# Optimization experiments

Hardware: AMD Instinct MI355X
Metric: run time of the kernel (lower is better)

## Reference

```python
import jax, jax.numpy as jnp
import numpy as np

N_LEVELS = 16
NFPL = 2
LOG2_T = 19
TABLE_SIZE = 1 << LOG2_T
BASE_RES = 16.0
FINEST_RES = 512.0
N_POINTS = 1048576

# hash primes from HashNeRF's hash() (xor of coord*prime per axis)
PRIMES = jnp.array([1, 2654435761, 805459861], dtype=jnp.uint32)
# corner offsets: index = 4*i + 2*j + k (i outermost), matching BOX_OFFSETS
OFFSETS = jnp.array([[i, j, k] for i in (0, 1) for j in (0, 1) for k in (0, 1)], dtype=jnp.int32)  # [8,3]


def setup_inputs() -> dict:
    key = jax.random.key(0)
    k1, k2 = jax.random.split(key)
    x = jax.random.uniform(k1, (N_POINTS, 3), dtype=jnp.float32)  # points in [0,1)^3
    # nn.Embedding tables init uniform(-1e-4, 1e-4), stacked over levels
    tables = jax.random.uniform(k2, (N_LEVELS, TABLE_SIZE, NFPL), minval=-1e-4, maxval=1e-4, dtype=jnp.float32)
    return {"x": x, "tables": tables}


def _level_embed(x, table, resolution):
    # x: [N,3] in box [0,1]^3; table: [T,F]; resolution: scalar float
    grid = 1.0 / resolution
    xc = jnp.clip(x, 0.0, 1.0)
    bl = jnp.floor(xc / grid).astype(jnp.int32)            # [N,3] bottom-left voxel idx
    vmin = bl.astype(jnp.float32) * grid                    # voxel_min_vertex
    vmax = vmin + grid                                      # voxel_max_vertex
    corners = bl[:, None, :] + OFFSETS[None, :, :]          # [N,8,3]
    h = corners.astype(jnp.uint32) * PRIMES                 # wrap-around uint32 mult
    idx = (h[..., 0] ^ h[..., 1] ^ h[..., 2]) & jnp.uint32(TABLE_SIZE - 1)  # [N,8]
    emb = table[idx.astype(jnp.int32)]                      # [N,8,F] gather
    # trilinear interp (weights use unclamped x as in the original)
    w = (x - vmin) / (vmax - vmin)                          # [N,3]
    w0, w1, w2 = w[:, 0:1], w[:, 1:2], w[:, 2:3]
    c00 = emb[:, 0] * (1 - w0) + emb[:, 4] * w0
    c01 = emb[:, 1] * (1 - w0) + emb[:, 5] * w0
    c10 = emb[:, 2] * (1 - w0) + emb[:, 6] * w0
    c11 = emb[:, 3] * (1 - w0) + emb[:, 7] * w0
    c0 = c00 * (1 - w1) + c10 * w1
    c1 = c01 * (1 - w1) + c11 * w1
    return c0 * (1 - w2) + c1 * w2                          # [N,F]


def reference(x, tables):
    b = np.exp((np.log(FINEST_RES) - np.log(BASE_RES)) / (N_LEVELS - 1))
    res = jnp.floor(BASE_RES * (b ** jnp.arange(N_LEVELS, dtype=jnp.float32)))  # [L]
    feats = jax.vmap(_level_embed, in_axes=(None, 0, 0))(x, tables, res)        # [L,N,F]
    out = jnp.moveaxis(feats, 0, 1).reshape(x.shape[0], N_LEVELS * NFPL)        # [N,32]
    # original: if last dim != 16, F.pad(x, (0, 16 - D)); negative pad crops
    D = out.shape[-1]
    if D > 16:
        out = out[:, :16]
    elif D < 16:
        out = jnp.pad(out, ((0, 0), (0, 16 - D)))
    return out
```

## Files before the change

### kernel.cpp

```cpp
#include <hip/hip_runtime.h>
#include <hip/hip_fp16.h>
#include <stdint.h>


#define TABLE_SIZE (1u << 19)
#define TMASK (TABLE_SIZE - 1u)
#define P2 2654435761u
#define P3 805459861u

#define FSCALE 8192.0f
#define FINV   1.220703125e-4f

#define QUAD_BYTES_OFF 262144
#define PAIR_BYTES_OFF 16777216

#define OFF_Q3 0
#define OFF_Q4 33792
#define OFF_Q5 99392
#define OFF_Q6 226892

__device__ __forceinline__ void quad_geom(int l, float& R, int& DK, int& offq) {
    switch (l) {
        case 3: R=32.f; DK=32; offq=OFF_Q3; break;
        case 4: R=40.f; DK=40; offq=OFF_Q4; break;
        case 5: R=50.f; DK=50; offq=OFF_Q5; break;
        default:R=64.f; DK=64; offq=OFF_Q6; break;
    }
}

__device__ __forceinline__ uint32_t pack_s(float a, float b) {
    __half2 h = __floats2half2_rn(a * FSCALE, b * FSCALE);
    return *(uint32_t*)&h;
}
__device__ __forceinline__ uint32_t pack_r(float a, float b) {
    __half2 h = __floats2half2_rn(a, b);
    return *(uint32_t*)&h;
}
__device__ __forceinline__ float2 h2f(uint32_t u) {
    __half2 h = *(__half2*)&u;
    return __half22float2(h);
}
__device__ __forceinline__ uint32_t getc(const uint4 v, int k) {
    return k == 0 ? v.x : k == 1 ? v.y : k == 2 ? v.z : v.w;
}

__global__ __launch_bounds__(256) void build_tables_kernel(
    const float* __restrict__ tables, float2* __restrict__ dense,
    uint4* __restrict__ quads, uint2* __restrict__ pairs)
{
    const int role = (int)blockIdx.y;
    const int e = (int)blockIdx.x * 256 + (int)threadIdx.x;

    if (role < 4) {
        float Rf; int DK, offq;
        quad_geom(3 + role, Rf, DK, offq);
        const int l = 3 + role;
        const int E = (DK + 1) * DK * DK;
        if (e >= E) return;
        const int d2 = DK * DK;
        const int i = e / d2;
        const int rem = e - i * d2;
        const int j = rem / DK;
        const int k = rem - j * DK;
        const float2* __restrict__ tab = (const float2*)tables + (size_t)l * (size_t)TABLE_SIZE;
        const uint32_t hx  = (uint32_t)i;
        const uint32_t hy0 = (uint32_t)j * P2, hy1 = hy0 + P2;
        const uint32_t hz0 = (uint32_t)k * P3, hz1 = hz0 + P3;
        const float2 v00 = tab[(hx ^ hy0 ^ hz0) & TMASK];
        const float2 v01 = tab[(hx ^ hy0 ^ hz1) & TMASK];
        const float2 v10 = tab[(hx ^ hy1 ^ hz0) & TMASK];
        const float2 v11 = tab[(hx ^ hy1 ^ hz1) & TMASK];
        uint4 u;
        u.x = pack_s(v00.x, v00.y);
        u.y = pack_s(v01.x, v01.y);
        u.z = pack_s(v10.x, v10.y);
        u.w = pack_s(v11.x, v11.y);
        quads[offq + e] = u;
    } else if (role == 4) {
        const int E = 81 * 81 * 80;
        if (e >= E) return;
        const int i = e / 6480;
        const int rem = e - i * 6480;
        const int j = rem / 80;
        const int k = rem - j * 80;
        const float2* __restrict__ tab = (const float2*)tables + (size_t)7 * (size_t)TABLE_SIZE;
        const uint32_t hb = (uint32_t)i ^ ((uint32_t)j * P2);
        const float2 a = tab[(hb ^ ((uint32_t)k * P3)) & TMASK];
        const float2 b = tab[(hb ^ ((uint32_t)(k + 1) * P3)) & TMASK];
        uint2 u;
        u.x = pack_s(a.x, a.y);
        u.y = pack_s(b.x, b.y);
        pairs[e] = u;
    } else {
        if (e >= 31750) return;
        int lv, DIM, off;
        if (e < 4913)       { lv = 0; DIM = 17; off = 0; }
        else if (e < 14174) { lv = 1; DIM = 21; off = 4913; }
        else                { lv = 2; DIM = 26; off = 14174; }
        const int le = e - off;
        const int d2 = DIM * DIM;
        const int i = le / d2;
        const int rem = le - i * d2;
        const int j = rem / DIM;
        const int k = rem - j * DIM;
        const uint32_t h = ((uint32_t)i ^ ((uint32_t)j * P2) ^ ((uint32_t)k * P3)) & TMASK;
        const float2* __restrict__ tab = (const float2*)tables + (size_t)lv * (size_t)TABLE_SIZE;
        dense[e] = tab[h];
    }
}

__device__ uint32_t embed_quad_one(int l, const uint4* __restrict__ quads,
                                   float px, float py, float pz) {
    float R; int DK, offq;
    quad_geom(l, R, DK, offq);
    const float g = 1.0f / R;
    const float cx = fminf(fmaxf(px, 0.0f), 1.0f);
    const float cy = fminf(fmaxf(py, 0.0f), 1.0f);
    const float cz = fminf(fmaxf(pz, 0.0f), 1.0f);
    const int bx = min((int)floorf(cx * R), DK - 1);
    const int by = min((int)floorf(cy * R), DK - 1);
    const int bz = min((int)floorf(cz * R), DK - 1);
    const float wx = (px - (float)bx * g) * R;
    const float wy = (py - (float)by * g) * R;
    const float wz = (pz - (float)bz * g) * R;
    const int d2 = DK * DK;
    const int idx = (bx * DK + by) * DK + bz;
    const uint4 qa = quads[offq + idx];
    const uint4 qb = quads[offq + idx + d2];
    const float omx = 1.0f - wx, omy = 1.0f - wy, omz = 1.0f - wz;
    const float2 a00 = h2f(qa.x), a01 = h2f(qa.y), a10 = h2f(qa.z), a11 = h2f(qa.w);
    const float2 b00 = h2f(qb.x), b01 = h2f(qb.y), b10 = h2f(qb.z), b11 = h2f(qb.w);
    const float m00a = a00.x*omx + b00.x*wx, m00b = a00.y*omx + b00.y*wx;
    const float m01a = a01.x*omx + b01.x*wx, m01b = a01.y*omx + b01.y*wx;
    const float m10a = a10.x*omx + b10.x*wx, m10b = a10.y*omx + b10.y*wx;
    const float m11a = a11.x*omx + b11.x*wx, m11b = a11.y*omx + b11.y*wx;
    const float c0a = m00a*omz + m01a*wz, c0b = m00b*omz + m01b*wz;
    const float c1a = m10a*omz + m11a*wz, c1b = m10b*omz + m11b*wz;
    return pack_r(c0a*omy + c1a*wy, c0b*omy + c1b*wy);
}
__device__ uint32_t embed_pair7_one(const uint2* __restrict__ pairs,
                                    float px, float py, float pz) {
    const float R = 80.f, g = 1.0f / R;
    const float cx = fminf(fmaxf(px, 0.0f), 1.0f);
    const float cy = fminf(fmaxf(py, 0.0f), 1.0f);
    const float cz = fminf(fmaxf(pz, 0.0f), 1.0f);
    const int bx = min((int)floorf(cx * R), 79);
    const int by = min((int)floorf(cy * R), 79);
    const int bz = min((int)floorf(cz * R), 79);
    const float wx = (px - (float)bx * g) * R;
    const float wy = (py - (float)by * g) * R;
    const float wz = (pz - (float)bz * g) * R;
    const int idx = (bx * 81 + by) * 80 + bz;
    const uint2 d00 = pairs[idx];
    const uint2 d01 = pairs[idx + 80];
    const uint2 d10 = pairs[idx + 6480];
    const uint2 d11 = pairs[idx + 6560];
    const float omx = 1.0f - wx, omy = 1.0f - wy, omz = 1.0f - wz;
    const float2 a00 = h2f(d00.x), z00 = h2f(d00.y);
    const float2 a01 = h2f(d01.x), z01 = h2f(d01.y);
    const float2 a10 = h2f(d10.x), z10 = h2f(d10.y);
    const float2 a11 = h2f(d11.x), z11 = h2f(d11.y);
    const float c00a = a00.x*omz + z00.x*wz, c00b = a00.y*omz + z00.y*wz;
    const float c01a = a01.x*omz + z01.x*wz, c01b = a01.y*omz + z01.y*wz;
    const float c10a = a10.x*omz + z10.x*wz, c10b = a10.y*omz + z10.y*wz;
    const float c11a = a11.x*omz + z11.x*wz, c11b = a11.y*omz + z11.y*wz;
    const float e0a = c00a*omy + c01a*wy, e0b = c00b*omy + c01b*wy;
    const float e1a = c10a*omy + c11a*wy, e1b = c10b*omy + c11b*wy;
    return pack_r(e0a*omx + e1a*wx, e0b*omx + e1b*wx);
}

__global__ __launch_bounds__(256, 4) void embed_levels_kernel(
    const float* __restrict__ x, const uint4* __restrict__ quads,
    const uint2* __restrict__ pairs, uint32_t* __restrict__ wsh,
    int n, int bpl)
{
    const int bid = (int)blockIdx.x;
    const int q = bid / bpl;
    const int l = 3 + q;
    const int pb = bid - q * bpl;
    const int p0 = pb * 1024 + 4 * (int)threadIdx.x;
    if (p0 >= n) return;

    uint32_t* __restrict__ wl = wsh + (size_t)l * (size_t)n;

    if (p0 + 4 > n) {
        for (int pp = 0; pp < 4; ++pp) {
            const int i = p0 + pp;
            if (i >= n) break;
            const float px = x[3*i], py = x[3*i+1], pz = x[3*i+2];
            wl[i] = (l < 7) ? embed_quad_one(l, quads, px, py, pz)
                            : embed_pair7_one(pairs, px, py, pz);
        }
        return;
    }

    const float4* __restrict__ xv = (const float4*)(x + (size_t)3 * p0);
    const float4 f0 = xv[0], f1 = xv[1], f2 = xv[2];
    const float px0 = f0.x, py0 = f0.y, pz0 = f0.z;
    const float px1 = f0.w, py1 = f1.x, pz1 = f1.y;
    const float px2 = f1.z, py2 = f1.w, pz2 = f2.x;
    const float px3 = f2.y, py3 = f2.z, pz3 = f2.w;

    uint32_t r0, r1, r2, r3;

    if (l < 7) {
        float R; int DK, offq;
        quad_geom(l, R, DK, offq);
        const float g = 1.0f / R;
        const int bmax = DK - 1;
        const int d2 = DK * DK;
        const uint4* __restrict__ tab = quads + offq;

#define QPREP(k) \
        const float cx##k = fminf(fmaxf(px##k, 0.0f), 1.0f); \
        const float cy##k = fminf(fmaxf(py##k, 0.0f), 1.0f); \
        const float cz##k = fminf(fmaxf(pz##k, 0.0f), 1.0f); \
        const int bx##k = min((int)floorf(cx##k * R), bmax); \
        const int by##k = min((int)floorf(cy##k * R), bmax); \
        const int bz##k = min((int)floorf(cz##k * R), bmax); \
        const float wx##k = (px##k - (float)bx##k * g) * R; \
        const float wy##k = (py##k - (float)by##k * g) * R; \
        const float wz##k = (pz##k - (float)bz##k * g) * R; \
        const int ia##k = (bx##k * DK + by##k) * DK + bz##k; \
        const int ib##k = ia##k + d2;

        QPREP(0) QPREP(1) QPREP(2) QPREP(3)

#define QGATHER(k) \
        const uint4 qa##k = tab[ia##k]; \
        const uint4 qb##k = tab[ib##k];

        QGATHER(0) QGATHER(1) QGATHER(2) QGATHER(3)

#define QINTERP(k, dst) { \
        const float omx = 1.0f - wx##k, omy = 1.0f - wy##k, omz = 1.0f - wz##k; \
        const float2 a00 = h2f(qa##k.x), a01 = h2f(qa##k.y); \
        const float2 a10 = h2f(qa##k.z), a11 = h2f(qa##k.w); \
        const float2 b00 = h2f(qb##k.x), b01 = h2f(qb##k.y); \
        const float2 b10 = h2f(qb##k.z), b11 = h2f(qb##k.w); \
        const float m00a = a00.x*omx + b00.x*wx##k, m00b = a00.y*omx + b00.y*wx##k; \
        const float m01a = a01.x*omx + b01.x*wx##k, m01b = a01.y*omx + b01.y*wx##k; \
        const float m10a = a10.x*omx + b10.x*wx##k, m10b = a10.y*omx + b10.y*wx##k; \
        const float m11a = a11.x*omx + b11.x*wx##k, m11b = a11.y*omx + b11.y*wx##k; \
        const float c0a = m00a*omz + m01a*wz##k, c0b = m00b*omz + m01b*wz##k; \
        const float c1a = m10a*omz + m11a*wz##k, c1b = m10b*omz + m11b*wz##k; \
        dst = pack_r(c0a*omy + c1a*wy##k, c0b*omy + c1b*wy##k); }

        QINTERP(0, r0) QINTERP(1, r1) QINTERP(2, r2) QINTERP(3, r3)
    } else {
        const float R = 80.f, g = 1.0f / R;

#define SPREP(k) \
        const float cx##k = fminf(fmaxf(px##k, 0.0f), 1.0f); \
        const float cy##k = fminf(fmaxf(py##k, 0.0f), 1.0f); \
        const float cz##k = fminf(fmaxf(pz##k, 0.0f), 1.0f); \
        const int bx##k = min((int)floorf(cx##k * R), 79); \
        const int by##k = min((int)floorf(cy##k * R), 79); \
        const int bz##k = min((int)floorf(cz##k * R), 79); \
        const float wx##k = (px##k - (float)bx##k * g) * R; \
        const float wy##k = (py##k - (float)by##k * g) * R; \
        const float wz##k = (pz##k - (float)bz##k * g) * R; \
        const int ix##k = (bx##k * 81 + by##k) * 80 + bz##k;

        SPREP(0) SPREP(1) SPREP(2) SPREP(3)

#define SGATHER(k) \
        const uint2 d00##k = pairs[ix##k]; \
        const uint2 d01##k = pairs[ix##k + 80]; \
        const uint2 d10##k = pairs[ix##k + 6480]; \
        const uint2 d11##k = pairs[ix##k + 6560];

        SGATHER(0) SGATHER(1) SGATHER(2) SGATHER(3)

#define SINTERP(k, dst) { \
        const float omx = 1.0f - wx##k, omy = 1.0f - wy##k, omz = 1.0f - wz##k; \
        const float2 a00 = h2f(d00##k.x), z00 = h2f(d00##k.y); \
        const float2 a01 = h2f(d01##k.x), z01 = h2f(d01##k.y); \
        const float2 a10 = h2f(d10##k.x), z10 = h2f(d10##k.y); \
        const float2 a11 = h2f(d11##k.x), z11 = h2f(d11##k.y); \
        const float c00a = a00.x*omz + z00.x*wz##k, c00b = a00.y*omz + z00.y*wz##k; \
        const float c01a = a01.x*omz + z01.x*wz##k, c01b = a01.y*omz + z01.y*wz##k; \
        const float c10a = a10.x*omz + z10.x*wz##k, c10b = a10.y*omz + z10.y*wz##k; \
        const float c11a = a11.x*omz + z11.x*wz##k, c11b = a11.y*omz + z11.y*wz##k; \
        const float e0a = c00a*omy + c01a*wy##k, e0b = c00b*omy + c01b*wy##k; \
        const float e1a = c10a*omy + c11a*wy##k, e1b = c10b*omy + c11b*wy##k; \
        dst = pack_r(e0a*omx + e1a*wx##k, e0b*omx + e1b*wx##k); }

        SINTERP(0, r0) SINTERP(1, r1) SINTERP(2, r2) SINTERP(3, r3)
    }

    *(uint4*)(wl + p0) = make_uint4(r0, r1, r2, r3);
}

__global__ __launch_bounds__(1024) void embed_lds_kernel(
    const float* __restrict__ x, const float2* __restrict__ dense,
    uint32_t* __restrict__ wsh, int n, int lv, int DIM, int E, int doff)
{
    extern __shared__ float2 lds[];
    for (int e = (int)threadIdx.x; e < E; e += 1024) lds[e] = dense[doff + e];
    __syncthreads();

    const int p0 = ((int)blockIdx.x * 1024 + (int)threadIdx.x) * 4;
    if (p0 >= n) return;

    const float R = (lv == 0) ? 16.f : (lv == 1) ? 20.f : 25.f;
    const float g = 1.0f / R;
    const int D2 = DIM * DIM;
    const int bmax = DIM - 2;

    float px[4], py[4], pz[4];
    if (p0 + 4 <= n) {
        const float4* __restrict__ xv = (const float4*)(x + (size_t)3 * p0);
        const float4 f0 = xv[0], f1 = xv[1], f2 = xv[2];
        px[0] = f0.x; py[0] = f0.y; pz[0] = f0.z;
        px[1] = f0.w; py[1] = f1.x; pz[1] = f1.y;
        px[2] = f1.z; py[2] = f1.w; pz[2] = f2.x;
        px[3] = f2.y; py[3] = f2.z; pz[3] = f2.w;
    } else {
#pragma unroll
        for (int k = 0; k < 4; ++k) {
            const int i = min(p0 + k, n - 1);
            px[k] = x[3*i]; py[k] = x[3*i+1]; pz[k] = x[3*i+2];
        }
    }

    uint32_t r[4];
#pragma unroll
    for (int k = 0; k < 4; ++k) {
        const float cx = fminf(fmaxf(px[k], 0.0f), 1.0f);
        const float cy = fminf(fmaxf(py[k], 0.0f), 1.0f);
        const float cz = fminf(fmaxf(pz[k], 0.0f), 1.0f);
        const int bx = min((int)floorf(cx * R), bmax);
        const int by = min((int)floorf(cy * R), bmax);
        const int bz = min((int)floorf(cz * R), bmax);
        const float wx = (px[k] - (float)bx * g) * R;
        const float wy = (py[k] - (float)by * g) * R;
        const float wz = (pz[k] - (float)bz * g) * R;
        const int c = (bx * DIM + by) * DIM + bz;
        const float2 e000 = lds[c];
        const float2 e001 = lds[c + 1];
        const float2 e010 = lds[c + DIM];
        const float2 e011 = lds[c + DIM + 1];
        const float2 e100 = lds[c + D2];
        const float2 e101 = lds[c + D2 + 1];
        const float2 e110 = lds[c + D2 + DIM];
        const float2 e111 = lds[c + D2 + DIM + 1];
        const float omx = 1.0f - wx, omy = 1.0f - wy, omz = 1.0f - wz;
        const float c00a = e000.x*omx + e100.x*wx, c00b = e000.y*omx + e100.y*wx;
        const float c01a = e001.x*omx + e101.x*wx, c01b = e001.y*omx + e101.y*wx;
        const float c10a = e010.x*omx + e110.x*wx, c10b = e010.y*omx + e110.y*wx;
        const float c11a = e011.x*omx + e111.x*wx, c11b = e011.y*omx + e111.y*wx;
        const float c0a = c00a*omy + c10a*wy, c0b = c00b*omy + c10b*wy;
        const float c1a = c01a*omy + c11a*wy, c1b = c01b*omy + c11b*wy;
        r[k] = pack_s(c0a*omz + c1a*wz, c0b*omz + c1b*wz);
    }
    if (p0 + 4 <= n) {
        *(uint4*)(wsh + (size_t)lv * n + p0) = make_uint4(r[0], r[1], r[2], r[3]);
    } else {
        for (int k = 0; k < 4 && p0 + k < n; ++k)
            wsh[(size_t)lv * n + p0 + k] = r[k];
    }
}

__global__ __launch_bounds__(256) void aos_kernel(
    const uint32_t* __restrict__ wsh, float* __restrict__ out, int n)
{
    const int p0 = ((int)blockIdx.x * 256 + (int)threadIdx.x) * 4;
    if (p0 >= n) return;

    if (p0 + 4 <= n) {
        const uint4 v0 = *(const uint4*)(wsh + 0 * (size_t)n + p0);
        const uint4 v1 = *(const uint4*)(wsh + 1 * (size_t)n + p0);
        const uint4 v2 = *(const uint4*)(wsh + 2 * (size_t)n + p0);
        const uint4 v3 = *(const uint4*)(wsh + 3 * (size_t)n + p0);
        const uint4 v4 = *(const uint4*)(wsh + 4 * (size_t)n + p0);
        const uint4 v5 = *(const uint4*)(wsh + 5 * (size_t)n + p0);
        const uint4 v6 = *(const uint4*)(wsh + 6 * (size_t)n + p0);
        const uint4 v7 = *(const uint4*)(wsh + 7 * (size_t)n + p0);
#pragma unroll
        for (int k = 0; k < 4; ++k) {
            const float2 f0 = h2f(getc(v0, k)), f1 = h2f(getc(v1, k));
            const float2 f2 = h2f(getc(v2, k)), f3 = h2f(getc(v3, k));
            const float2 f4 = h2f(getc(v4, k)), f5 = h2f(getc(v5, k));
            const float2 f6 = h2f(getc(v6, k)), f7 = h2f(getc(v7, k));
            float4* __restrict__ op = (float4*)(out + (size_t)(p0 + k) * 16);
            op[0] = make_float4(f0.x*FINV, f0.y*FINV, f1.x*FINV, f1.y*FINV);
            op[1] = make_float4(f2.x*FINV, f2.y*FINV, f3.x*FINV, f3.y*FINV);
            op[2] = make_float4(f4.x*FINV, f4.y*FINV, f5.x*FINV, f5.y*FINV);
            op[3] = make_float4(f6.x*FINV, f6.y*FINV, f7.x*FINV, f7.y*FINV);
        }
    } else {
        for (int k = 0; k < 4 && p0 + k < n; ++k) {
            const int i = p0 + k;
            float* __restrict__ op = out + (size_t)i * 16;
#pragma unroll
            for (int l = 0; l < 8; ++l) {
                const float2 f = h2f(wsh[(size_t)l * n + i]);
                op[2*l + 0] = f.x * FINV;
                op[2*l + 1] = f.y * FINV;
            }
        }
    }
}

__global__ __launch_bounds__(256) void hash_embed_mono_kernel(
    const float* __restrict__ x, const float* __restrict__ tables,
    float* __restrict__ out, int n)
{
    const int i = blockIdx.x * 256 + threadIdx.x;
    if (i >= n) return;
    const float px = x[3*i+0], py = x[3*i+1], pz = x[3*i+2];
    const float cx = fminf(fmaxf(px, 0.0f), 1.0f);
    const float cy = fminf(fmaxf(py, 0.0f), 1.0f);
    const float cz = fminf(fmaxf(pz, 0.0f), 1.0f);
    const float resf[8] = {16.f,20.f,25.f,32.f,40.f,50.f,64.f,80.f};
    float o[16];
#pragma unroll
    for (int l = 0; l < 8; ++l) {
        const float R = resf[l], g = 1.0f / R;
        const int bx = (int)floorf(cx*R), by = (int)floorf(cy*R), bz = (int)floorf(cz*R);
        const float wx = (px - bx*g)*R, wy = (py - by*g)*R, wz = (pz - bz*g)*R;
        const uint32_t hx0 = (uint32_t)bx, hx1 = hx0+1u;
        const uint32_t hy0 = (uint32_t)by*P2, hy1 = hy0+P2;
        const uint32_t hz0 = (uint32_t)bz*P3, hz1 = hz0+P3;
        const float2* tab = (const float2*)(tables) + (size_t)l*(size_t)TABLE_SIZE;
        const float2 e000 = tab[(hx0^hy0^hz0)&TMASK], e001 = tab[(hx0^hy0^hz1)&TMASK];
        const float2 e010 = tab[(hx0^hy1^hz0)&TMASK], e011 = tab[(hx0^hy1^hz1)&TMASK];
        const float2 e100 = tab[(hx1^hy0^hz0)&TMASK], e101 = tab[(hx1^hy0^hz1)&TMASK];
        const float2 e110 = tab[(hx1^hy1^hz0)&TMASK], e111 = tab[(hx1^hy1^hz1)&TMASK];
        const float omx = 1.f-wx, omy = 1.f-wy, omz = 1.f-wz;
        const float c00a = e000.x*omx + e100.x*wx, c00b = e000.y*omx + e100.y*wx;
        const float c01a = e001.x*omx + e101.x*wx, c01b = e001.y*omx + e101.y*wx;
        const float c10a = e010.x*omx + e110.x*wx, c10b = e010.y*omx + e110.y*wx;
        const float c11a = e011.x*omx + e111.x*wx, c11b = e011.y*omx + e111.y*wx;
        const float c0a = c00a*omy + c10a*wy, c0b = c00b*omy + c10b*wy;
        const float c1a = c01a*omy + c11a*wy, c1b = c01b*omy + c11b*wy;
        o[2*l+0] = c0a*omz + c1a*wz;
        o[2*l+1] = c0b*omz + c1b*wz;
    }
    float4* op = (float4*)(out + (size_t)i * 16);
    op[0] = make_float4(o[0],o[1],o[2],o[3]);
    op[1] = make_float4(o[4],o[5],o[6],o[7]);
    op[2] = make_float4(o[8],o[9],o[10],o[11]);
    op[3] = make_float4(o[12],o[13],o[14],o[15]);
}

extern "C" void kernel_launch(void* const* d_in, const int* in_sizes, int n_in,
                              void* d_out, int out_size, void* d_ws, size_t ws_size,
                              hipStream_t stream) {
    const float* x = (const float*)d_in[0];
    const float* tables = (const float*)d_in[1];
    float* out = (float*)d_out;
    const int n = in_sizes[0] / 3;

    static int cap = -1;
    if (cap < 0) {
        cap = (hipFuncSetAttribute((const void*)embed_lds_kernel,
                  hipFuncAttributeMaxDynamicSharedMemorySize, 140608) == hipSuccess)
              ? 1 : 0;
    }
    const size_t ws_needed = (size_t)8 * (size_t)n * sizeof(uint32_t);
    if (ws_size < ws_needed || cap == 0) {
        hash_embed_mono_kernel<<<(n + 255) / 256, 256, 0, stream>>>(x, tables, out, n);
        return;
    }

    uint32_t* wsh = (uint32_t*)d_ws;
    float2* dense = (float2*)out;
    uint4*  quads = (uint4*)((char*)out + QUAD_BYTES_OFF);
    uint2*  pairs = (uint2*)((char*)out + PAIR_BYTES_OFF);

    build_tables_kernel<<<dim3(2051, 6), 256, 0, stream>>>(tables, dense, quads, pairs);

    static const int DIMt[3] = {17, 21, 26};
    static const int Et[3]   = {4913, 9261, 17576};
    static const int OFFt[3] = {0, 4913, 14174};
    const int lgrid = (n + 4095) / 4096;
    for (int lv = 0; lv < 3; ++lv) {
        embed_lds_kernel<<<lgrid, 1024, (size_t)Et[lv] * sizeof(float2), stream>>>(
            x, dense, wsh, n, lv, DIMt[lv], Et[lv], OFFt[lv]);
    }

    const int bpl = (n + 1023) / 1024;
    embed_levels_kernel<<<5 * bpl, 256, 0, stream>>>(x, quads, pairs, wsh, n, bpl);

    aos_kernel<<<(n + 1023) / 1024, 256, 0, stream>>>(wsh, out, n);
}
```

Before: 255.5 us.

## Fuse coarse dense levels into output kernel and move level 2 to quad path

```diff
diff --git a/kernel.cpp b/kernel.cpp
--- a/kernel.cpp
+++ b/kernel.cpp
@@ -14,13 +14,19 @@
 #define QUAD_BYTES_OFF 262144
 #define PAIR_BYTES_OFF 16777216
 
-#define OFF_Q3 0
-#define OFF_Q4 33792
-#define OFF_Q5 99392
-#define OFF_Q6 226892
+#define OFF_Q2 0
+#define OFF_Q3 16250
+#define OFF_Q4 50042
+#define OFF_Q5 115642
+#define OFF_Q6 243142
+
+#define DENSE_L1_OFF 4913
+#define DENSE_E 14174
+#define DENSE_BYTES (DENSE_E * 8)
 
 __device__ __forceinline__ void quad_geom(int l, float& R, int& DK, int& offq) {
     switch (l) {
+        case 2: R=25.f; DK=25; offq=OFF_Q2; break;
         case 3: R=32.f; DK=32; offq=OFF_Q3; break;
         case 4: R=40.f; DK=40; offq=OFF_Q4; break;
         case 5: R=50.f; DK=50; offq=OFF_Q5; break;
@@ -51,10 +57,10 @@
     const int role = (int)blockIdx.y;
     const int e = (int)blockIdx.x * 256 + (int)threadIdx.x;
 
-    if (role < 4) {
+    if (role < 5) {
         float Rf; int DK, offq;
-        quad_geom(3 + role, Rf, DK, offq);
-        const int l = 3 + role;
+        quad_geom(2 + role, Rf, DK, offq);
+        const int l = 2 + role;
         const int E = (DK + 1) * DK * DK;
         if (e >= E) return;
         const int d2 = DK * DK;
@@ -76,7 +82,7 @@
         u.z = pack_s(v10.x, v10.y);
         u.w = pack_s(v11.x, v11.y);
         quads[offq + e] = u;
-    } else if (role == 4) {
+    } else if (role == 5) {
         const int E = 81 * 81 * 80;
         if (e >= E) return;
         const int i = e / 6480;
@@ -92,11 +98,10 @@
         u.y = pack_s(b.x, b.y);
         pairs[e] = u;
     } else {
-        if (e >= 31750) return;
+        if (e >= DENSE_E) return;
         int lv, DIM, off;
-        if (e < 4913)       { lv = 0; DIM = 17; off = 0; }
-        else if (e < 14174) { lv = 1; DIM = 21; off = 4913; }
-        else                { lv = 2; DIM = 26; off = 14174; }
+        if (e < 4913) { lv = 0; DIM = 17; off = 0; }
+        else          { lv = 1; DIM = 21; off = 4913; }
         const int le = e - off;
         const int d2 = DIM * DIM;
         const int i = le / d2;
@@ -176,7 +181,7 @@
 {
     const int bid = (int)blockIdx.x;
     const int q = bid / bpl;
-    const int l = 3 + q;
+    const int l = 2 + q;
     const int pb = bid - q * bpl;
     const int p0 = pb * 1024 + 4 * (int)threadIdx.x;
     if (p0 >= n) return;
@@ -292,21 +297,17 @@
     *(uint4*)(wl + p0) = make_uint4(r0, r1, r2, r3);
 }
 
-__global__ __launch_bounds__(1024) void embed_lds_kernel(
-    const float* __restrict__ x, const float2* __restrict__ dense,
-    uint32_t* __restrict__ wsh, int n, int lv, int DIM, int E, int doff)
+__global__ __launch_bounds__(1024) void final_kernel(
+    const float* __restrict__ x, const uint32_t* wsh,
+    float* __restrict__ out, int n)
 {
     extern __shared__ float2 lds[];
-    for (int e = (int)threadIdx.x; e < E; e += 1024) lds[e] = dense[doff + e];
+    const float2* dense = (const float2*)wsh;
+    for (int e = (int)threadIdx.x; e < DENSE_E; e += 1024) lds[e] = dense[e];
     __syncthreads();
 
     const int p0 = ((int)blockIdx.x * 1024 + (int)threadIdx.x) * 4;
     if (p0 >= n) return;
-
-    const float R = (lv == 0) ? 16.f : (lv == 1) ? 20.f : 25.f;
-    const float g = 1.0f / R;
-    const int D2 = DIM * DIM;
-    const int bmax = DIM - 2;
 
     float px[4], py[4], pz[4];
     if (p0 + 4 <= n) {
@@ -324,82 +325,75 @@
         }
     }
 
-    uint32_t r[4];
+    uint4 v[6];
+    if (p0 + 4 <= n) {
+#pragma unroll
+        for (int l = 0; l < 6; ++l)
+            v[l] = *(const uint4*)(wsh + (size_t)(l + 2) * n + p0);
+    } else {
+#pragma unroll
+        for (int l = 0; l < 6; ++l) {
+            uint4 t;
+            t.x = wsh[(size_t)(l+2)*n + min(p0+0, n-1)];
+            t.y = wsh[(size_t)(l+2)*n + min(p0+1, n-1)];
+            t.z = wsh[(size_t)(l+2)*n + min(p0+2, n-1)];
+            t.w = wsh[(size_t)(l+2)*n + min(p0+3, n-1)];
+            v[l] = t;
+        }
+    }
+
+    float l0a[4], l0b[4], l1a[4], l1b[4];
 #pragma unroll
     for (int k = 0; k < 4; ++k) {
-        const float cx = fminf(fmaxf(px[k], 0.0f), 1.0f);
-        const float cy = fminf(fmaxf(py[k], 0.0f), 1.0f);
-        const float cz = fminf(fmaxf(pz[k], 0.0f), 1.0f);
-        const int bx = min((int)floorf(cx * R), bmax);
-        const int by = min((int)floorf(cy * R), bmax);
-        const int bz = min((int)floorf(cz * R), bmax);
-        const float wx = (px[k] - (float)bx * g) * R;
-        const float wy = (py[k] - (float)by * g) * R;
-        const float wz = (pz[k] - (float)bz * g) * R;
-        const int c = (bx * DIM + by) * DIM + bz;
-        const float2 e000 = lds[c];
-        const float2 e001 = lds[c + 1];
-        const float2 e010 = lds[c + DIM];
-        const float2 e011 = lds[c + DIM + 1];
-        const float2 e100 = lds[c + D2];
-        const float2 e101 = lds[c + D2 + 1];
-        const float2 e110 = lds[c + D2 + DIM];
-        const float2 e111 = lds[c + D2 + DIM + 1];
-        const float omx = 1.0f - wx, omy = 1.0f - wy, omz = 1.0f - wz;
-        const float c00a = e000.x*omx + e100.x*wx, c00b = e000.y*omx + e100.y*wx;
-        const float c01a = e001.x*omx + e101.x*wx, c01b = e001.y*omx + e101.y*wx;
-        const float c10a = e010.x*omx + e110.x*wx, c10b = e010.y*omx + e110.y*wx;
-        const float c11a = e011.x*omx + e111.x*wx, c11b = e011.y*omx + e111.y*wx;
-        const float c0a = c00a*omy + c10a*wy, c0b = c00b*omy + c10b*wy;
-        const float c1a = c01a*omy + c11a*wy, c1b = c01b*omy + c11b*wy;
-        r[k] = pack_s(c0a*omz + c1a*wz, c0b*omz + c1b*wz);
-    }
-    if (p0 + 4 <= n) {
-        *(uint4*)(wsh + (size_t)lv * n + p0) = make_uint4(r[0], r[1], r[2], r[3]);
-    } else {
-        for (int k = 0; k < 4 && p0 + k < n; ++k)
-            wsh[(size_t)lv * n + p0 + k] = r[k];
-    }
-}
-
-__global__ __launch_bounds__(256) void aos_kernel(
-    const uint32_t* __restrict__ wsh, float* __restrict__ out, int n)
-{
-    const int p0 = ((int)blockIdx.x * 256 + (int)threadIdx.x) * 4;
-    if (p0 >= n) return;
-
-    if (p0 + 4 <= n) {
-        const uint4 v0 = *(const uint4*)(wsh + 0 * (size_t)n + p0);
-        const uint4 v1 = *(const uint4*)(wsh + 1 * (size_t)n + p0);
-        const uint4 v2 = *(const uint4*)(wsh + 2 * (size_t)n + p0);
-        const uint4 v3 = *(const uint4*)(wsh + 3 * (size_t)n + p0);
-        const uint4 v4 = *(const uint4*)(wsh + 4 * (size_t)n + p0);
-        const uint4 v5 = *(const uint4*)(wsh + 5 * (size_t)n + p0);
-        const uint4 v6 = *(const uint4*)(wsh + 6 * (size_t)n + p0);
-        const uint4 v7 = *(const uint4*)(wsh + 7 * (size_t)n + p0);
-#pragma unroll
-        for (int k = 0; k < 4; ++k) {
-            const float2 f0 = h2f(getc(v0, k)), f1 = h2f(getc(v1, k));
-            const float2 f2 = h2f(getc(v2, k)), f3 = h2f(getc(v3, k));
-            const float2 f4 = h2f(getc(v4, k)), f5 = h2f(getc(v5, k));
-            const float2 f6 = h2f(getc(v6, k)), f7 = h2f(getc(v7, k));
-            float4* __restrict__ op = (float4*)(out + (size_t)(p0 + k) * 16);
-            op[0] = make_float4(f0.x*FINV, f0.y*FINV, f1.x*FINV, f1.y*FINV);
-            op[1] = make_float4(f2.x*FINV, f2.y*FINV, f3.x*FINV, f3.y*FINV);
-            op[2] = make_float4(f4.x*FINV, f4.y*FINV, f5.x*FINV, f5.y*FINV);
-            op[3] = make_float4(f6.x*FINV, f6.y*FINV, f7.x*FINV, f7.y*FINV);
+#pragma unroll
+        for (int lv = 0; lv < 2; ++lv) {
+            const float R = (lv == 0) ? 16.f : 20.f;
+            const int DIM = (lv == 0) ? 17 : 21;
+            const int off = (lv == 0) ? 0 : DENSE_L1_OFF;
+            const float g = 1.0f / R;
+            const int D2 = DIM * DIM;
+            const int bmax = DIM - 2;
+            const float cx = fminf(fmaxf(px[k], 0.0f), 1.0f);
+            const float cy = fminf(fmaxf(py[k], 0.0f), 1.0f);
+            const float cz = fminf(fmaxf(pz[k], 0.0f), 1.0f);
+            const int bx = min((int)floorf(cx * R), bmax);
+            const int by = min((int)floorf(cy * R), bmax);
+            const int bz = min((int)floorf(cz * R), bmax);
+            const float wx = (px[k] - (float)bx * g) * R;
+            const float wy = (py[k] - (float)by * g) * R;
+            const float wz = (pz[k] - (float)bz * g) * R;
+            const int c = off + (bx * DIM + by) * DIM + bz;
+            const float2 e000 = lds[c];
+            const float2 e001 = lds[c + 1];
+            const float2 e010 = lds[c + DIM];
+            const float2 e011 = lds[c + DIM + 1];
+            const float2 e100 = lds[c + D2];
+            const float2 e101 = lds[c + D2 + 1];
+            const float2 e110 = lds[c + D2 + DIM];
+            const float2 e111 = lds[c + D2 + DIM + 1];
+            const float omx = 1.0f - wx, omy = 1.0f - wy, omz = 1.0f - wz;
+            const float c00a = e000.x*omx + e100.x*wx, c00b = e000.y*omx + e100.y*wx;
+            const float c01a = e001.x*omx + e101.x*wx, c01b = e001.y*omx + e101.y*wx;
+            const float c10a = e010.x*omx + e110.x*wx, c10b = e010.y*omx + e110.y*wx;
+            const float c11a = e011.x*omx + e111.x*wx, c11b = e011.y*omx + e111.y*wx;
+            const float c0a = c00a*omy + c10a*wy, c0b = c00b*omy + c10b*wy;
+            const float c1a = c01a*omy + c11a*wy, c1b = c01b*omy + c11b*wy;
+            if (lv == 0) { l0a[k] = c0a*omz + c1a*wz; l0b[k] = c0b*omz + c1b*wz; }
+            else         { l1a[k] = c0a*omz + c1a*wz; l1b[k] = c0b*omz + c1b*wz; }
         }
-    } else {
-        for (int k = 0; k < 4 && p0 + k < n; ++k) {
-            const int i = p0 + k;
-            float* __restrict__ op = out + (size_t)i * 16;
-#pragma unroll
-            for (int l = 0; l < 8; ++l) {
-                const float2 f = h2f(wsh[(size_t)l * n + i]);
-                op[2*l + 0] = f.x * FINV;
-                op[2*l + 1] = f.y * FINV;
-            }
-        }
+    }
+
+#pragma unroll
+    for (int k = 0; k < 4; ++k) {
+        if (p0 + k >= n) break;
+        const float2 f2v = h2f(getc(v[0], k)), f3v = h2f(getc(v[1], k));
+        const float2 f4v = h2f(getc(v[2], k)), f5v = h2f(getc(v[3], k));
+        const float2 f6v = h2f(getc(v[4], k)), f7v = h2f(getc(v[5], k));
+        float4* __restrict__ op = (float4*)(out + (size_t)(p0 + k) * 16);
+        op[0] = make_float4(l0a[k], l0b[k], l1a[k], l1b[k]);
+        op[1] = make_float4(f2v.x*FINV, f2v.y*FINV, f3v.x*FINV, f3v.y*FINV);
+        op[2] = make_float4(f4v.x*FINV, f4v.y*FINV, f5v.x*FINV, f5v.y*FINV);
+        op[3] = make_float4(f6v.x*FINV, f6v.y*FINV, f7v.x*FINV, f7v.y*FINV);
     }
 }
 
@@ -455,8 +449,8 @@
 
     static int cap = -1;
     if (cap < 0) {
-        cap = (hipFuncSetAttribute((const void*)embed_lds_kernel,
-                  hipFuncAttributeMaxDynamicSharedMemorySize, 140608) == hipSuccess)
+        cap = (hipFuncSetAttribute((const void*)final_kernel,
+                  hipFuncAttributeMaxDynamicSharedMemorySize, DENSE_BYTES) == hipSuccess)
               ? 1 : 0;
     }
     const size_t ws_needed = (size_t)8 * (size_t)n * sizeof(uint32_t);
@@ -466,23 +460,14 @@
     }
 
     uint32_t* wsh = (uint32_t*)d_ws;
-    float2* dense = (float2*)out;
+    float2* dense = (float2*)d_ws;
     uint4*  quads = (uint4*)((char*)out + QUAD_BYTES_OFF);
     uint2*  pairs = (uint2*)((char*)out + PAIR_BYTES_OFF);
 
-    build_tables_kernel<<<dim3(2051, 6), 256, 0, stream>>>(tables, dense, quads, pairs);
-
-    static const int DIMt[3] = {17, 21, 26};
-    static const int Et[3]   = {4913, 9261, 17576};
-    static const int OFFt[3] = {0, 4913, 14174};
-    const int lgrid = (n + 4095) / 4096;
-    for (int lv = 0; lv < 3; ++lv) {
-        embed_lds_kernel<<<lgrid, 1024, (size_t)Et[lv] * sizeof(float2), stream>>>(
-            x, dense, wsh, n, lv, DIMt[lv], Et[lv], OFFt[lv]);
-    }
+    build_tables_kernel<<<dim3(2051, 7), 256, 0, stream>>>(tables, dense, quads, pairs);
 
     const int bpl = (n + 1023) / 1024;
-    embed_levels_kernel<<<5 * bpl, 256, 0, stream>>>(x, quads, pairs, wsh, n, bpl);
-
-    aos_kernel<<<(n + 1023) / 1024, 256, 0, stream>>>(wsh, out, n);
-}
+    embed_levels_kernel<<<6 * bpl, 256, 0, stream>>>(x, quads, pairs, wsh, n, bpl);
+
+    final_kernel<<<(n + 4095) / 4096, 1024, DENSE_BYTES, stream>>>(x, wsh, out, n);
+}
```

Result: faster. 228.7 us (-10.5%).
